# Kernel tuning notes

Measured on AMD Instinct MI355X. Metric: run time of the kernel, lower is better.

Reference implementation:

```python
import jax, jax.numpy as jnp
import numpy as np

C = 768
H = 12
T = 4096
B = 1
EPS = 1e-5


def setup_inputs() -> dict:
    key = jax.random.key(0)
    ks = jax.random.split(key, 16)
    s = 0.02
    return {
        "x": jax.random.normal(ks[0], (B, T, C), jnp.float32),
        "ln1_w": jnp.ones((C,), jnp.float32),
        "ln1_b": jnp.zeros((C,), jnp.float32),
        "W_attn": jax.random.normal(ks[1], (C, 3 * C), jnp.float32) * s,
        "b_attn": jnp.zeros((3 * C,), jnp.float32),
        "W_proj": jax.random.normal(ks[2], (C, C), jnp.float32) * s,
        "b_proj": jnp.zeros((C,), jnp.float32),
        "ln2_w": jnp.ones((C,), jnp.float32),
        "ln2_b": jnp.zeros((C,), jnp.float32),
        "W_fc": jax.random.normal(ks[3], (C, 4 * C), jnp.float32) * s,
        "b_fc": jnp.zeros((4 * C,), jnp.float32),
        "W_fc2": jax.random.normal(ks[4], (4 * C, C), jnp.float32) * s,
        "b_fc2": jnp.zeros((C,), jnp.float32),
    }


def _layernorm(x, w, b):
    mu = jnp.mean(x, axis=-1, keepdims=True)
    var = jnp.var(x, axis=-1, keepdims=True)
    return (x - mu) * jax.lax.rsqrt(var + EPS) * w + b


def _attn(x, W_attn, b_attn, W_proj, b_proj):
    Bb, Tt, Cc = x.shape
    hd = Cc // H
    qkv = x @ W_attn + b_attn                       # (B,T,3C)
    q, k, v = jnp.split(qkv, 3, axis=-1)
    q = q.reshape(Bb, Tt, H, hd).transpose(0, 2, 1, 3)  # (B,H,T,hd)
    k = k.reshape(Bb, Tt, H, hd).transpose(0, 2, 1, 3)
    v = v.reshape(Bb, Tt, H, hd).transpose(0, 2, 1, 3)
    att = jnp.einsum('bhqd,bhkd->bhqk', q, k) * (1.0 / np.sqrt(hd))
    causal = jnp.tril(jnp.ones((Tt, Tt), bool))
    att = jnp.where(causal, att, -jnp.inf)
    att = jax.nn.softmax(att, axis=-1)
    y = jnp.einsum('bhqk,bhkd->bhqd', att, v)       # (B,H,T,hd)
    y = y.transpose(0, 2, 1, 3).reshape(Bb, Tt, Cc)
    return y @ W_proj + b_proj


def _mlp(x, W_fc, b_fc, W_fc2, b_fc2):
    h = jax.nn.gelu(x @ W_fc + b_fc, approximate=False)
    return h @ W_fc2 + b_fc2


def reference(x, ln1_w, ln1_b, W_attn, b_attn, W_proj, b_proj,
              ln2_w, ln2_b, W_fc, b_fc, W_fc2, b_fc2):
    x = x + _attn(_layernorm(x, ln1_w, ln1_b), W_attn, b_attn, W_proj, b_proj)
    x = x + _mlp(_layernorm(x, ln2_w, ln2_b), W_fc, b_fc, W_fc2, b_fc2)
    return x
```

## Files before the change

### kernel.cpp

```cpp
#include <hip/hip_runtime.h>
#include <hip/hip_bf16.h>
#include <math.h>
#include <type_traits>

#define TSEQ 4096
#define CDIM 768
#define NH 12
#define HD 64

typedef float f32x4 __attribute__((ext_vector_type(4)));
typedef __bf16 bf16x8 __attribute__((ext_vector_type(8)));
typedef short s16x8 __attribute__((ext_vector_type(8)));
typedef uint u32x4 __attribute__((ext_vector_type(4)));

__device__ inline ushort f2bf(float f) {
  __hip_bfloat16 h = __float2bfloat16(f);
  return __builtin_bit_cast(ushort, h);
}

__device__ inline void async16(const void* g, void* l) {
  __builtin_amdgcn_global_load_lds(
      (__attribute__((address_space(1))) unsigned int*)(uintptr_t)g,
      (__attribute__((address_space(3))) unsigned int*)(uintptr_t)l, 16, 0, 0);
}

__device__ inline float exp2_fast(float x) {
  float r;
  asm volatile("v_exp_f32 %0, %1\n\ts_nop 0" : "=v"(r) : "v"(x));
  return r;
}

__device__ inline uint cvtpk(float a, float b) {
  uint r;
  asm volatile("v_cvt_pk_bf16_f32 %0, %1, %2" : "=v"(r) : "v"(a), "v"(b));
  return r;
}

__device__ inline bf16x8 frag_read(const ushort* base, int row, int kk, int lane) {
  const int byte = row * 128 + ((((kk * 4 + (lane >> 4)) ^ (row & 7))) << 4);
  return *(const bf16x8*)((const char*)base + byte);
}

__device__ void wconv_body(const float* __restrict__ W, ushort* __restrict__ Wt,
                           int K, int N, int bx, int by)
{
  __shared__ float sm[32][33];
  const int n0 = bx * 32, k0 = by * 32;
  const int c = threadIdx.x & 31, r0 = threadIdx.x >> 5;
#pragma unroll
  for (int i = 0; i < 4; ++i) {
    const int r = r0 + i * 8;
    sm[r][c] = W[(size_t)(k0 + r) * N + n0 + c];
  }
  __syncthreads();
#pragma unroll
  for (int i = 0; i < 4; ++i) {
    const int r = r0 + i * 8;
    Wt[(size_t)(n0 + r) * K + k0 + c] = f2bf(sm[c][r]);
  }
}

__device__ void ln_body(const float* __restrict__ x, const float* __restrict__ w,
                        const float* __restrict__ b, ushort* __restrict__ out, int row)
{
  const int tid = threadIdx.x;
  const float* xr = x + (size_t)row * CDIM;
  float v[3];
  float s1 = 0.f, s2 = 0.f;
#pragma unroll
  for (int i = 0; i < 3; ++i) {
    v[i] = xr[tid + i * 256];
    s1 += v[i];
    s2 += v[i] * v[i];
  }
#pragma unroll
  for (int off = 32; off >= 1; off >>= 1) {
    s1 += __shfl_xor(s1, off, 64);
    s2 += __shfl_xor(s2, off, 64);
  }
  __shared__ float red1[4], red2[4];
  if ((tid & 63) == 0) { red1[tid >> 6] = s1; red2[tid >> 6] = s2; }
  __syncthreads();
  s1 = red1[0] + red1[1] + red1[2] + red1[3];
  s2 = red2[0] + red2[1] + red2[2] + red2[3];
  const float mu = s1 * (1.f / CDIM);
  const float var = s2 * (1.f / CDIM) - mu * mu;
  const float inv = rsqrtf(var + 1e-5f);
#pragma unroll
  for (int i = 0; i < 3; ++i) {
    const int c2 = tid + i * 256;
    out[(size_t)row * CDIM + c2] = f2bf((v[i] - mu) * inv * w[c2] + b[c2]);
  }
}

__global__ __launch_bounds__(256) void prep_kernel(
    const float* __restrict__ W_attn, ushort* __restrict__ Wt_attn,
    const float* __restrict__ W_proj, ushort* __restrict__ Wt_proj,
    const float* __restrict__ W_fc,   ushort* __restrict__ Wt_fc,
    const float* __restrict__ W_fc2,  ushort* __restrict__ Wt_fc2,
    const float* __restrict__ x, const float* __restrict__ ln1w,
    const float* __restrict__ ln1b, ushort* __restrict__ t_ln)
{
  int b = blockIdx.x;
  if (b < 1728) { wconv_body(W_attn, Wt_attn, 768, 2304, b % 72, b / 72); return; }
  b -= 1728;
  if (b < 576)  { wconv_body(W_proj, Wt_proj, 768, 768, b % 24, b / 24); return; }
  b -= 576;
  if (b < 2304) { wconv_body(W_fc, Wt_fc, 768, 3072, b % 96, b / 96); return; }
  b -= 2304;
  if (b < 2304) { wconv_body(W_fc2, Wt_fc2, 3072, 768, b % 24, b / 24); return; }
  b -= 2304;
  ln_body(x, ln1w, ln1b, t_ln, b);
}

__global__ __launch_bounds__(256) void ln_kernel(
    const float* __restrict__ x, const float* __restrict__ w,
    const float* __restrict__ b, ushort* __restrict__ out)
{
  ln_body(x, w, b, out, blockIdx.x);
}

template <int EPI, int BN>
__global__ __launch_bounds__(256) void gemm_bt(
    const ushort* __restrict__ A, const ushort* __restrict__ Bt,
    const float* __restrict__ bias, const float* __restrict__ res,
    ushort* __restrict__ outb, float* __restrict__ outf,
    int M, int N, int K, int gx)
{
  constexpr int NW = BN / 32;
  __shared__ __align__(16) ushort As[3][128 * 32];
  __shared__ __align__(16) ushort Bs[3][BN * 32];
  const int tid = threadIdx.x;
  const int lane = tid & 63;
  const int wv = tid >> 6;
  const int nwg = (int)gridDim.x;
  const int bid = (int)blockIdx.x;
  const int sw = (bid & 7) * (nwg >> 3) + (bid >> 3);
  const int rowBase = (sw / gx) * 128;
  const int colBase = (sw % gx) * BN;
  const int wr = (wv >> 1) * 64;
  const int wc = (wv & 1) * (BN / 2);

  f32x4 acc[4][NW] = {};

  const int e0 = tid * 8;
  const int r0 = e0 >> 5, c0 = e0 & 31;
  const int e1 = (tid + 256) * 8;
  const int r1 = e1 >> 5, c1 = e1 & 31;

  const ushort* Ag0 = A + (size_t)(rowBase + r0) * K + c0;
  const ushort* Ag1 = A + (size_t)(rowBase + r1) * K + c1;
  const ushort* Bg0 = Bt + (size_t)(colBase + r0) * K + c0;
  const ushort* Bg1 = Bt + (size_t)(colBase + r1) * K + c1;

  auto stage = [&](int buf, int k0) {
    async16(Ag0 + k0, &As[buf][e0]);
    async16(Ag1 + k0, &As[buf][e1]);
    async16(Bg0 + k0, &Bs[buf][e0]);
    if (BN == 128) async16(Bg1 + k0, &Bs[buf][e1]);
  };

  const int nt = K / 32;
  stage(0, 0);
  stage(1, 32);
  int b0 = 0, b1 = 1, b2 = 2;
  for (int t = 0; t < nt; ++t) {
    if (t < nt - 1) {
      if (BN == 128) asm volatile("s_waitcnt vmcnt(4)" ::: "memory");
      else           asm volatile("s_waitcnt vmcnt(3)" ::: "memory");
    } else {
      asm volatile("s_waitcnt vmcnt(0)" ::: "memory");
    }
    __builtin_amdgcn_sched_barrier(0);
    __builtin_amdgcn_s_barrier();
    __builtin_amdgcn_sched_barrier(0);
    if (t + 2 < nt) stage(b2, t * 32 + 64);

    bf16x8 af[4], bfr[NW];
#pragma unroll
    for (int m = 0; m < 4; ++m)
      af[m] = *(const bf16x8*)&As[b0][(wr + m * 16 + (lane & 15)) * 32 + (lane >> 4) * 8];
#pragma unroll
    for (int n = 0; n < NW; ++n)
      bfr[n] = *(const bf16x8*)&Bs[b0][(wc + n * 16 + (lane & 15)) * 32 + (lane >> 4) * 8];
#pragma unroll
    for (int m = 0; m < 4; ++m)
#pragma unroll
      for (int n = 0; n < NW; ++n)
        acc[m][n] = __builtin_amdgcn_mfma_f32_16x16x32_bf16(af[m], bfr[n], acc[m][n], 0, 0, 0);
    const int tmp = b0; b0 = b1; b1 = b2; b2 = tmp;
  }

#pragma unroll
  for (int n = 0; n < NW; ++n) {
    const int gc = colBase + wc + n * 16 + (lane & 15);
    const float bv = bias[gc];
#pragma unroll
    for (int m = 0; m < 4; ++m) {
#pragma unroll
      for (int j = 0; j < 4; ++j) {
        const int gr = rowBase + wr + m * 16 + (lane >> 4) * 4 + j;
        const float v = acc[m][n][j] + bv;
        if (EPI == 0) {
          outb[(size_t)gr * N + gc] = f2bf(v);
        } else if (EPI == 1) {
          outf[(size_t)gr * N + gc] = res[(size_t)gr * N + gc] + v;
        } else {
          const float g = 0.5f * v * (1.0f + erff(v * 0.70710678118654752f));
          outb[(size_t)gr * N + gc] = f2bf(g);
        }
      }
    }
  }
}

__global__ __launch_bounds__(256) void attn_kernel(
    const ushort* __restrict__ qkv, ushort* __restrict__ att)
{
  __shared__ __align__(16) ushort Ks[2][64 * 64];
  __shared__ __align__(16) ushort Vt[2][64 * 64];

  const int tid = threadIdx.x;
  const int lane = tid & 63;
  const int wv = tid >> 6;
  const int g = lane >> 4;
  const int ql = lane & 15;
  const int kh = wv & 1;
  const int qh = wv >> 1;
  const int p_ = blockIdx.x & 255, grp = blockIdx.x >> 8;
  const int item = (grp & 1) ? (grp * 256 + 255 - p_) : (grp * 256 + p_);
  const int qb = 63 - (item / 12);
  const int h = item % 12;
  const int t0 = qb * 64;
  const size_t rs = 3 * CDIM;
  const int qo = h * HD, ko = CDIM + h * HD, vo = 2 * CDIM + h * HD;

  const float cexp = 0.18033688f;
  const float cbias = -32.0f * 0.18033688f;

  const int L0 = tid * 16, L1 = (tid + 256) * 16;
  const int r_0 = L0 >> 7, c_0 = ((L0 >> 4) & 7) ^ (r_0 & 7);
  const int r_1 = L1 >> 7, c_1 = ((L1 >> 4) & 7) ^ (r_1 & 7);
  const ushort* kg0 = qkv + (size_t)r_0 * rs + ko + c_0 * 8;
  const ushort* kg1 = qkv + (size_t)r_1 * rs + ko + c_1 * 8;

  const int vt = (tid >> 3) * 2;
  const int vd = (tid & 7) * 8;
  const int s32 = vt & 31;
  const int col2 = (vt >> 5) * 64 + (8 * ((s32 >> 2) & 3) + 4 * (s32 >> 4) + (s32 & 3)) * 2;
  const ushort* vg = qkv + (size_t)vt * rs + vo + vd;

  bf16x8 qf[2][2];
#pragma unroll
  for (int qg = 0; qg < 2; ++qg) {
    const ushort* qrow = qkv + (size_t)(t0 + 32 * qh + 16 * qg + ql) * rs + qo + g * 8;
    qf[qg][0] = *(const bf16x8*)(qrow);
    qf[qg][1] = *(const bf16x8*)(qrow + 32);
  }

  s16x8 vA0 = *(const s16x8*)(vg);
  s16x8 vA1 = *(const s16x8*)(vg + rs);
  async16(kg0, (char*)Ks[0] + L0);
  async16(kg1, (char*)Ks[0] + L1);
#pragma unroll
  for (int jj = 0; jj < 8; ++jj) {
    const int d = vd + jj;
    const uint val = (uint)(ushort)vA0[jj] | ((uint)(ushort)vA1[jj] << 16);
    *(uint*)((char*)Vt[0] + d * 128 + (col2 ^ (((d >> 1) & 7) << 4))) = val;
  }

  f32x4 accO[2][4] = {};
  f32x4 accL[2] = {};
  const bf16x8 ones = __builtin_bit_cast(bf16x8,
      (u32x4){0x3F803F80u, 0x3F803F80u, 0x3F803F80u, 0x3F803F80u});
  const int swzv = (ql >> 1) & 7;

  int cur = 0;
  auto body = [&](int kb, int curb, auto diag_c) {
    constexpr bool DIAG = decltype(diag_c)::value;
    const size_t koff = (size_t)(kb + 1) * 64 * rs;

    if (!DIAG) {
      vA0 = *(const s16x8*)(vg + koff);
      vA1 = *(const s16x8*)(vg + koff + rs);
      asm volatile("s_waitcnt vmcnt(2) lgkmcnt(0)" ::: "memory");
    } else {
      asm volatile("s_waitcnt vmcnt(0) lgkmcnt(0)" ::: "memory");
    }
    __builtin_amdgcn_sched_barrier(0);
    __builtin_amdgcn_s_barrier();
    __builtin_amdgcn_sched_barrier(0);

    if (!DIAG) {
      async16(kg0 + koff, (char*)Ks[curb ^ 1] + L0);
      async16(kg1 + koff, (char*)Ks[curb ^ 1] + L1);
    }

    f32x4 accS[2][2] = {};
#pragma unroll
    for (int kg = 0; kg < 2; ++kg)
#pragma unroll
      for (int kk = 0; kk < 2; ++kk) {
        const bf16x8 A = frag_read(Ks[curb], 32 * kh + 16 * kg + ql, kk, lane);
#pragma unroll
        for (int qg = 0; qg < 2; ++qg)
          accS[kg][qg] = __builtin_amdgcn_mfma_f32_16x16x32_bf16(
              A, qf[qg][kk], accS[kg][qg], 0, 0, 0);
      }

    bf16x8 pa[2];
#pragma unroll
    for (int qg = 0; qg < 2; ++qg) {
      float e[2][4];
#pragma unroll
      for (int kg = 0; kg < 2; ++kg)
#pragma unroll
        for (int j = 0; j < 4; ++j) {
          float s = exp2_fast(fmaf(accS[kg][qg][j], cexp, cbias));
          if (DIAG && (32 * kh + 16 * kg + 4 * g + j) > (32 * qh + 16 * qg + ql)) s = 0.f;
          e[kg][j] = s;
        }
      const uint w0 = cvtpk(e[0][0], e[0][1]);
      const uint w1 = cvtpk(e[0][2], e[0][3]);
      const uint w2 = cvtpk(e[1][0], e[1][1]);
      const uint w3 = cvtpk(e[1][2], e[1][3]);
      pa[qg] = __builtin_bit_cast(bf16x8, (u32x4){w0, w1, w2, w3});
    }

#pragma unroll
    for (int n = 0; n < 4; ++n) {
      const int byte = (16 * n + ql) * 128 + ((kh * 64 + 16 * g) ^ (swzv << 4));
      const bf16x8 bv = *(const bf16x8*)((const char*)Vt[curb] + byte);
#pragma unroll
      for (int qg = 0; qg < 2; ++qg)
        accO[qg][n] = __builtin_amdgcn_mfma_f32_16x16x32_bf16(pa[qg], bv, accO[qg][n], 0, 0, 0);
    }
#pragma unroll
    for (int qg = 0; qg < 2; ++qg)
      accL[qg] = __builtin_amdgcn_mfma_f32_16x16x32_bf16(pa[qg], ones, accL[qg], 0, 0, 0);

    if (!DIAG) {
#pragma unroll
      for (int jj = 0; jj < 8; ++jj) {
        const int d = vd + jj;
        const uint val = (uint)(ushort)vA0[jj] | ((uint)(ushort)vA1[jj] << 16);
        *(uint*)((char*)Vt[curb ^ 1] + d * 128 + (col2 ^ (((d >> 1) & 7) << 4))) = val;
      }
    }
  };

  for (int kb = 0; kb < qb; ++kb) {
    body(kb, cur, std::false_type{});
    cur ^= 1;
  }
  body(qb, cur, std::true_type{});

  __syncthreads();
  float* mO = (float*)&Ks[0][0];
  float* mL = (float*)&Vt[0][0];
  if (kh == 1) {
#pragma unroll
    for (int qg = 0; qg < 2; ++qg) {
#pragma unroll
      for (int n = 0; n < 4; ++n)
        *(f32x4*)&mO[(((qh * 2 + qg) * 4 + n) * 64 + lane) * 4] = accO[qg][n];
      *(f32x4*)&mL[((qh * 2 + qg) * 64 + lane) * 4] = accL[qg];
    }
  }
  __syncthreads();
  if (kh == 0) {
#pragma unroll
    for (int qg = 0; qg < 2; ++qg) {
      const f32x4 ls = accL[qg] + *(const f32x4*)&mL[((qh * 2 + qg) * 64 + lane) * 4];
      f32x4 inv4;
#pragma unroll
      for (int jr = 0; jr < 4; ++jr) inv4[jr] = 1.0f / ls[jr];
#pragma unroll
      for (int n = 0; n < 4; ++n) {
        const f32x4 o = accO[qg][n] +
            *(const f32x4*)&mO[(((qh * 2 + qg) * 4 + n) * 64 + lane) * 4];
#pragma unroll
        for (int jr = 0; jr < 4; ++jr) {
          const int tq = t0 + 32 * qh + 16 * qg + 4 * g + jr;
          const int d = 16 * n + ql;
          att[(size_t)tq * CDIM + h * HD + d] = f2bf(o[jr] * inv4[jr]);
        }
      }
    }
  }
}

extern "C" void kernel_launch(void* const* d_in, const int* in_sizes, int n_in,
                              void* d_out, int out_size, void* d_ws, size_t ws_size,
                              hipStream_t stream)
{
  const float* x      = (const float*)d_in[0];
  const float* ln1_w  = (const float*)d_in[1];
  const float* ln1_b  = (const float*)d_in[2];
  const float* W_attn = (const float*)d_in[3];
  const float* b_attn = (const float*)d_in[4];
  const float* W_proj = (const float*)d_in[5];
  const float* b_proj = (const float*)d_in[6];
  const float* ln2_w  = (const float*)d_in[7];
  const float* ln2_b  = (const float*)d_in[8];
  const float* W_fc   = (const float*)d_in[9];
  const float* b_fc   = (const float*)d_in[10];
  const float* W_fc2  = (const float*)d_in[11];
  const float* b_fc2  = (const float*)d_in[12];
  float* out = (float*)d_out;

  char* base = (char*)d_ws;
  size_t off = 0;
  auto alloc = [&](size_t bytes) -> void* {
    void* q = base + off;
    off = (off + bytes + 255) & ~(size_t)255;
    return q;
  };
  ushort* Wt_attn = (ushort*)alloc(768ull * 2304 * 2);
  ushort* Wt_proj = (ushort*)alloc(768ull * 768 * 2);
  ushort* Wt_fc   = (ushort*)alloc(768ull * 3072 * 2);
  ushort* Wt_fc2  = (ushort*)alloc(3072ull * 768 * 2);
  ushort* t_ln    = (ushort*)alloc(4096ull * 768 * 2);
  ushort* t_att   = (ushort*)alloc(4096ull * 768 * 2);
  float*  t_x1    = (float*) alloc(4096ull * 768 * 4);
  ushort* t_big   = (ushort*)alloc(4096ull * 3072 * 2);
  ushort* t_qkv = t_big;
  ushort* t_h   = t_big;

  prep_kernel<<<11008, 256, 0, stream>>>(
      W_attn, Wt_attn, W_proj, Wt_proj, W_fc, Wt_fc, W_fc2, Wt_fc2,
      x, ln1_w, ln1_b, t_ln);
  gemm_bt<0, 128><<<18 * 32, 256, 0, stream>>>(
      t_ln, Wt_attn, b_attn, nullptr, t_qkv, nullptr, 4096, 2304, 768, 18);
  attn_kernel<<<dim3(768), 256, 0, stream>>>(t_qkv, t_att);
  gemm_bt<1, 64><<<12 * 32, 256, 0, stream>>>(
      t_att, Wt_proj, b_proj, x, nullptr, t_x1, 4096, 768, 768, 12);
  ln_kernel<<<4096, 256, 0, stream>>>(t_x1, ln2_w, ln2_b, t_ln);
  gemm_bt<2, 128><<<24 * 32, 256, 0, stream>>>(
      t_ln, Wt_fc, b_fc, nullptr, t_h, nullptr, 4096, 3072, 768, 24);
  gemm_bt<1, 64><<<12 * 32, 256, 0, stream>>>(
      t_h, Wt_fc2, b_fc2, t_x1, nullptr, out, 4096, 768, 3072, 12);
}
```

Before: 189.1 us.

## Split-K the projection and FC2 GEMMs with atomic accumulation

```diff
diff --git a/kernel.cpp b/kernel.cpp
--- a/kernel.cpp
+++ b/kernel.cpp
@@ -99,7 +99,8 @@
     const float* __restrict__ W_fc,   ushort* __restrict__ Wt_fc,
     const float* __restrict__ W_fc2,  ushort* __restrict__ Wt_fc2,
     const float* __restrict__ x, const float* __restrict__ ln1w,
-    const float* __restrict__ ln1b, ushort* __restrict__ t_ln)
+    const float* __restrict__ ln1b, ushort* __restrict__ t_ln,
+    float* __restrict__ zero1, float* __restrict__ zero2)
 {
   int b = blockIdx.x;
   if (b < 1728) { wconv_body(W_attn, Wt_attn, 768, 2304, b % 72, b / 72); return; }
@@ -110,7 +111,14 @@
   b -= 2304;
   if (b < 2304) { wconv_body(W_fc2, Wt_fc2, 3072, 768, b % 24, b / 24); return; }
   b -= 2304;
-  ln_body(x, ln1w, ln1b, t_ln, b);
+  if (b < 4096) { ln_body(x, ln1w, ln1b, t_ln, b); return; }
+  b -= 4096;
+  float* dst = (b < 768) ? zero1 : zero2;
+  const int bb = (b < 768) ? b : b - 768;
+  const f32x4 z = {0.f, 0.f, 0.f, 0.f};
+#pragma unroll
+  for (int i = 0; i < 4; ++i)
+    *(f32x4*)&dst[((size_t)bb * 1024 + i * 256 + threadIdx.x) * 4] = z;
 }
 
 __global__ __launch_bounds__(256) void ln_kernel(
@@ -125,7 +133,7 @@
     const ushort* __restrict__ A, const ushort* __restrict__ Bt,
     const float* __restrict__ bias, const float* __restrict__ res,
     ushort* __restrict__ outb, float* __restrict__ outf,
-    int M, int N, int K, int gx)
+    int M, int N, int K, int gx, int Kstride)
 {
   constexpr int NW = BN / 32;
   __shared__ __align__(16) ushort As[3][128 * 32];
@@ -135,11 +143,17 @@
   const int wv = tid >> 6;
   const int nwg = (int)gridDim.x;
   const int bid = (int)blockIdx.x;
-  const int sw = (bid & 7) * (nwg >> 3) + (bid >> 3);
+  int sw = (bid & 7) * (nwg >> 3) + (bid >> 3);
+  int kh = 0;
+  if (EPI == 3) {
+    const int half = nwg >> 1;
+    if (sw >= half) { kh = 1; sw -= half; }
+  }
   const int rowBase = (sw / gx) * 128;
   const int colBase = (sw % gx) * BN;
   const int wr = (wv >> 1) * 64;
   const int wc = (wv & 1) * (BN / 2);
+  const int koffK = kh * K;
 
   f32x4 acc[4][NW] = {};
 
@@ -148,10 +162,10 @@
   const int e1 = (tid + 256) * 8;
   const int r1 = e1 >> 5, c1 = e1 & 31;
 
-  const ushort* Ag0 = A + (size_t)(rowBase + r0) * K + c0;
-  const ushort* Ag1 = A + (size_t)(rowBase + r1) * K + c1;
-  const ushort* Bg0 = Bt + (size_t)(colBase + r0) * K + c0;
-  const ushort* Bg1 = Bt + (size_t)(colBase + r1) * K + c1;
+  const ushort* Ag0 = A + (size_t)(rowBase + r0) * Kstride + koffK + c0;
+  const ushort* Ag1 = A + (size_t)(rowBase + r1) * Kstride + koffK + c1;
+  const ushort* Bg0 = Bt + (size_t)(colBase + r0) * Kstride + koffK + c0;
+  const ushort* Bg1 = Bt + (size_t)(colBase + r1) * Kstride + koffK + c1;
 
   auto stage = [&](int buf, int k0) {
     async16(Ag0 + k0, &As[buf][e0]);
@@ -200,14 +214,20 @@
 #pragma unroll
       for (int j = 0; j < 4; ++j) {
         const int gr = rowBase + wr + m * 16 + (lane >> 4) * 4 + j;
-        const float v = acc[m][n][j] + bv;
+        const size_t idx = (size_t)gr * N + gc;
+        const float v = acc[m][n][j];
         if (EPI == 0) {
-          outb[(size_t)gr * N + gc] = f2bf(v);
+          outb[idx] = f2bf(v + bv);
         } else if (EPI == 1) {
-          outf[(size_t)gr * N + gc] = res[(size_t)gr * N + gc] + v;
+          outf[idx] = res[idx] + v + bv;
+        } else if (EPI == 2) {
+          const float vb = v + bv;
+          const float g = 0.5f * vb * (1.0f + erff(vb * 0.70710678118654752f));
+          outb[idx] = f2bf(g);
         } else {
-          const float g = 0.5f * v * (1.0f + erff(v * 0.70710678118654752f));
-          outb[(size_t)gr * N + gc] = f2bf(g);
+          float add = v;
+          if (kh == 0) add += bv + res[idx];
+          atomicAdd(&outf[idx], add);
         }
       }
     }
@@ -297,6 +317,7 @@
     }
 
     f32x4 accS[2][2] = {};
+    __builtin_amdgcn_s_setprio(1);
 #pragma unroll
     for (int kg = 0; kg < 2; ++kg)
 #pragma unroll
@@ -307,6 +328,7 @@
           accS[kg][qg] = __builtin_amdgcn_mfma_f32_16x16x32_bf16(
               A, qf[qg][kk], accS[kg][qg], 0, 0, 0);
       }
+    __builtin_amdgcn_s_setprio(0);
 
     bf16x8 pa[2];
 #pragma unroll
@@ -327,6 +349,7 @@
       pa[qg] = __builtin_bit_cast(bf16x8, (u32x4){w0, w1, w2, w3});
     }
 
+    __builtin_amdgcn_s_setprio(1);
 #pragma unroll
     for (int n = 0; n < 4; ++n) {
       const int byte = (16 * n + ql) * 128 + ((kh * 64 + 16 * g) ^ (swzv << 4));
@@ -338,6 +361,7 @@
 #pragma unroll
     for (int qg = 0; qg < 2; ++qg)
       accL[qg] = __builtin_amdgcn_mfma_f32_16x16x32_bf16(pa[qg], ones, accL[qg], 0, 0, 0);
+    __builtin_amdgcn_s_setprio(0);
 
     if (!DIAG) {
 #pragma unroll
@@ -427,17 +451,17 @@
   ushort* t_qkv = t_big;
   ushort* t_h   = t_big;
 
-  prep_kernel<<<11008, 256, 0, stream>>>(
+  prep_kernel<<<12544, 256, 0, stream>>>(
       W_attn, Wt_attn, W_proj, Wt_proj, W_fc, Wt_fc, W_fc2, Wt_fc2,
-      x, ln1_w, ln1_b, t_ln);
+      x, ln1_w, ln1_b, t_ln, out, t_x1);
   gemm_bt<0, 128><<<18 * 32, 256, 0, stream>>>(
-      t_ln, Wt_attn, b_attn, nullptr, t_qkv, nullptr, 4096, 2304, 768, 18);
+      t_ln, Wt_attn, b_attn, nullptr, t_qkv, nullptr, 4096, 2304, 768, 18, 768);
   attn_kernel<<<dim3(768), 256, 0, stream>>>(t_qkv, t_att);
-  gemm_bt<1, 64><<<12 * 32, 256, 0, stream>>>(
-      t_att, Wt_proj, b_proj, x, nullptr, t_x1, 4096, 768, 768, 12);
+  gemm_bt<3, 64><<<2 * 12 * 32, 256, 0, stream>>>(
+      t_att, Wt_proj, b_proj, x, nullptr, t_x1, 4096, 768, 384, 12, 768);
   ln_kernel<<<4096, 256, 0, stream>>>(t_x1, ln2_w, ln2_b, t_ln);
   gemm_bt<2, 128><<<24 * 32, 256, 0, stream>>>(
-      t_ln, Wt_fc, b_fc, nullptr, t_h, nullptr, 4096, 3072, 768, 24);
-  gemm_bt<1, 64><<<12 * 32, 256, 0, stream>>>(
-      t_h, Wt_fc2, b_fc2, t_x1, nullptr, out, 4096, 768, 3072, 12);
-}
+      t_ln, Wt_fc, b_fc, nullptr, t_h, nullptr, 4096, 3072, 768, 24, 768);
+  gemm_bt<3, 64><<<2 * 12 * 32, 256, 0, stream>>>(
+      t_h, Wt_fc2, b_fc2, t_x1, nullptr, out, 4096, 768, 1536, 12, 3072);
+}
```

Result: slower. 218.3 us (+15.5%).
